# Kernel optimization log

Hardware: AMD Instinct MI355X
Metric: run time of the kernel (lower is better)

## Reference

```python
import jax, jax.numpy as jnp
import numpy as np

L = 2          # num encoder layers
D = 256        # node_dim / d_model
H = 4          # nhead
FF = 4 * D     # dim_feedforward
GEO = 8        # geo feature dim (bi ++ bj)
HID = 512      # relation MLP hidden
C = 56         # num_rel_classes
N = 384        # number of nodes


def layer_norm(x, g, b, eps=1e-5):
    mu = jnp.mean(x, axis=-1, keepdims=True)
    var = jnp.mean((x - mu) ** 2, axis=-1, keepdims=True)
    return (x - mu) * jax.lax.rsqrt(var + eps) * g + b


def encoder_layer(x, wi, bi, wo, bo, w1, b1, w2, b2, g1, be1, g2, be2):
    # Post-norm torch TransformerEncoderLayer (norm_first=False, relu)
    n = x.shape[0]
    dh = D // H
    qkv = x @ wi + bi                                  # [n, 3D]
    q, k, v = jnp.split(qkv, 3, axis=-1)
    q = q.reshape(n, H, dh)
    k = k.reshape(n, H, dh)
    v = v.reshape(n, H, dh)
    scores = jnp.einsum('nhd,mhd->hnm', q, k) * (dh ** -0.5)
    attn = jax.nn.softmax(scores, axis=-1)
    o = jnp.einsum('hnm,mhd->nhd', attn, v).reshape(n, D) @ wo + bo
    x = layer_norm(x + o, g1, be1)
    f = jax.nn.relu(x @ w1 + b1) @ w2 + b2
    x = layer_norm(x + f, g2, be2)
    return x


def setup_inputs() -> dict:
    key = jax.random.key(0)
    ks = jax.random.split(key, 16)
    s = 0.02
    f32 = jnp.float32
    return {
        'node_feats': jax.random.normal(ks[0], (N, D), f32),
        'boxes_norm': jax.random.uniform(ks[1], (N, 4), dtype=f32),
        'attn_w_in': jax.random.normal(ks[2], (L, D, 3 * D), f32) * s,
        'attn_b_in': jnp.zeros((L, 3 * D), f32),
        'attn_w_out': jax.random.normal(ks[3], (L, D, D), f32) * s,
        'attn_b_out': jnp.zeros((L, D), f32),
        'ffn_w1': jax.random.normal(ks[4], (L, D, FF), f32) * s,
        'ffn_b1': jnp.zeros((L, FF), f32),
        'ffn_w2': jax.random.normal(ks[5], (L, FF, D), f32) * s,
        'ffn_b2': jnp.zeros((L, D), f32),
        'ln1_g': jnp.ones((L, D), f32),
        'ln1_b': jnp.zeros((L, D), f32),
        'ln2_g': jnp.ones((L, D), f32),
        'ln2_b': jnp.zeros((L, D), f32),
        'mlp_w1': jax.random.normal(ks[6], (2 * D + GEO, HID), f32) * s,
        'mlp_b1': jnp.zeros((HID,), f32),
        'mlp_w2': jax.random.normal(ks[7], (HID, C), f32) * s,
        'mlp_b2': jnp.zeros((C,), f32),
    }


def reference(node_feats, boxes_norm, attn_w_in, attn_b_in, attn_w_out,
              attn_b_out, ffn_w1, ffn_b1, ffn_w2, ffn_b2, ln1_g, ln1_b,
              ln2_g, ln2_b, mlp_w1, mlp_b1, mlp_w2, mlp_b2):
    x = node_feats
    for l in range(L):
        x = encoder_layer(x, attn_w_in[l], attn_b_in[l], attn_w_out[l],
                          attn_b_out[l], ffn_w1[l], ffn_b1[l], ffn_w2[l],
                          ffn_b2[l], ln1_g[l], ln1_b[l], ln2_g[l], ln2_b[l])
    n = node_feats.shape[0]
    # all ordered pairs (i, j), i != j, in row-major order matching the loop
    i_full = np.repeat(np.arange(n), n)
    j_full = np.tile(np.arange(n), n)
    keep = i_full != j_full
    idx_i = jnp.asarray(i_full[keep])
    idx_j = jnp.asarray(j_full[keep])
    rel_in = jnp.concatenate(
        [x[idx_i], x[idx_j], boxes_norm[idx_i], boxes_norm[idx_j]], axis=1)
    rel_logits = jax.nn.relu(rel_in @ mlp_w1 + mlp_b1) @ mlp_w2 + mlp_b2
    pair_idx = jnp.stack([idx_i, idx_j], axis=1)
    return (pair_idx, rel_logits)
```

## Files before the change

### kernel.cpp

```cpp
#include <hip/hip_runtime.h>

#define NN 384
#define DM 256
#define NH 4
#define FF 1024
#define HIDN 512
#define NCLS 56
#define NPAIR (NN*(NN-1))

typedef __attribute__((ext_vector_type(8))) short short8v;
typedef __attribute__((ext_vector_type(4))) float f32x4;
typedef __attribute__((ext_vector_type(16))) float f32x16;
typedef __attribute__((ext_vector_type(8))) unsigned short ushort8;
typedef __attribute__((ext_vector_type(4))) unsigned int uint4v;

static __device__ __forceinline__ unsigned short f2bf(float f) {
  unsigned u = __float_as_uint(f);
  unsigned r = u + 0x7fff + ((u >> 16) & 1);
  return (unsigned short)(r >> 16);
}
static __device__ __forceinline__ float bf2f(unsigned short v) {
  return __uint_as_float(((unsigned)v) << 16);
}
static __device__ __forceinline__ unsigned cvt_pk_bf16(float lo, float hi) {
  unsigned r;
  asm("v_cvt_pk_bf16_f32 %0, %1, %2" : "=v"(r) : "v"(lo), "v"(hi));
  return r;
}
#define MLROW(reg, half) (((reg) & 3) + 8 * ((reg) >> 2) + 4 * (half))

__global__ __launch_bounds__(256)
void pack_all(const float* __restrict__ wi, const float* __restrict__ wo,
              const float* __restrict__ w1, const float* __restrict__ w2,
              const float* __restrict__ mw1, const float* __restrict__ mw2,
              unsigned short* __restrict__ wi_f, unsigned short* __restrict__ wo_f,
              unsigned short* __restrict__ w1_f, unsigned short* __restrict__ w2_f,
              unsigned short* __restrict__ mw1_f, unsigned short* __restrict__ mw2_f) {
  int y = blockIdx.y, z = blockIdx.z;
  int t = blockIdx.x * 256 + threadIdx.x;
  const float* src; unsigned short* dst; int K, N; long sS, sD;
  switch (y) {
    case 0: src = wi;  dst = wi_f;  K = 256;  N = 768;  sS = 256L*768;  sD = 196608; break;
    case 1: src = wo;  dst = wo_f;  K = 256;  N = 256;  sS = 256L*256;  sD = 65536;  break;
    case 2: src = w1;  dst = w1_f;  K = 256;  N = 1024; sS = 256L*1024; sD = 262144; break;
    case 3: src = w2;  dst = w2_f;  K = 1024; N = 256;  sS = 1024L*256; sD = 262144; break;
    case 4: src = mw1; dst = mw1_f; K = 256;  N = 512;  sS = 256L*512;  sD = 131072; break;
    default: {
      if (z || t >= 4096) return;
      int l = t & 63, nt = (t >> 6) & 1, ks = t >> 7;
      int kb = ks * 16 + ((l >> 5) * 8), n = nt * 32 + (l & 31);
      #pragma unroll
      for (int r = 0; r < 8; ++r) {
        float v = (n < NCLS) ? mw2[(size_t)(kb + r) * NCLS + n] : 0.f;
        mw2_f[(size_t)t * 8 + r] = f2bf(v);
      }
      return;
    }
  }
  int Nt = N >> 5;
  int total = (K >> 4) * Nt * 64;
  if (t >= total) return;
  src += z * sS; dst += z * sD;
  int l = t & 63;
  int rem = t >> 6;
  int nt = rem % Nt, ks = rem / Nt;
  int kb = ks * 16 + ((l >> 5) * 8), n = nt * 32 + (l & 31);
  #pragma unroll
  for (int r = 0; r < 8; ++r)
    dst[(size_t)t * 8 + r] = f2bf(src[(size_t)(kb + r) * N + n]);
}

__global__ __launch_bounds__(256)
void x_init(const float* __restrict__ node, float* __restrict__ xbuf,
            unsigned short* __restrict__ xbf) {
  int i = blockIdx.x * 256 + threadIdx.x;
  float v = node[i];
  xbuf[i] = v;
  xbf[i] = f2bf(v);
}

__global__ __launch_bounds__(128)
void qkv_mfma(const unsigned short* __restrict__ xbf, const unsigned short* __restrict__ wif,
              const float* __restrict__ bi, unsigned short* __restrict__ qk,
              unsigned short* __restrict__ vt) {
  int id = blockIdx.x * 2 + (threadIdx.x >> 6);
  int lane = threadIdx.x & 63;
  int mt = id % 12, nt = id / 12;
  int col = lane & 31, half = lane >> 5;
  const unsigned short* asrc = xbf + (size_t)(mt * 32 + col) * 256 + half * 8;
  const unsigned short* bsrc = wif + ((size_t)nt * 64 + lane) * 8;
  f32x16 acc = {};
  #pragma unroll
  for (int ks = 0; ks < 16; ++ks) {
    short8v a = *reinterpret_cast<const short8v*>(asrc + ks * 16);
    short8v b = *reinterpret_cast<const short8v*>(bsrc + (size_t)ks * 24 * 512);
    acc = __builtin_amdgcn_mfma_f32_32x32x16_bf16(a, b, acc, 0, 0, 0);
  }
  int n = nt * 32 + col;
  float bb = bi[n];
  #pragma unroll
  for (int reg = 0; reg < 16; ++reg) {
    int row = mt * 32 + MLROW(reg, half);
    float v = acc[reg] + bb;
    if (n < 512) qk[(size_t)row * 512 + n] = f2bf(v);
    else         vt[(size_t)(n - 512) * 384 + row] = f2bf(v);
  }
}

__global__ __launch_bounds__(256)
void fused_attn(const unsigned short* __restrict__ qk, const unsigned short* __restrict__ vt,
                unsigned short* __restrict__ attno) {
  __shared__ float S[32][385];
  __shared__ unsigned short P[32][392];
  int n0 = blockIdx.x * 32;
  int h = blockIdx.y;
  int wave = threadIdx.x >> 6, lane = threadIdx.x & 63;
  int col = lane & 31, half = lane >> 5;
  {
    const unsigned short* asrc = qk + (size_t)(n0 + col) * 512 + h * 64 + half * 8;
    #pragma unroll
    for (int jj = 0; jj < 3; ++jj) {
      int ntk = wave * 3 + jj;
      const unsigned short* bsrc = qk + (size_t)(ntk * 32 + col) * 512 + 256 + h * 64 + half * 8;
      f32x16 acc = {};
      #pragma unroll
      for (int ks = 0; ks < 4; ++ks) {
        short8v a = *reinterpret_cast<const short8v*>(asrc + ks * 16);
        short8v b = *reinterpret_cast<const short8v*>(bsrc + ks * 16);
        acc = __builtin_amdgcn_mfma_f32_32x32x16_bf16(a, b, acc, 0, 0, 0);
      }
      #pragma unroll
      for (int reg = 0; reg < 16; ++reg)
        S[MLROW(reg, half)][ntk * 32 + col] = acc[reg] * 0.125f;
    }
  }
  __syncthreads();
  {
    int row = threadIdx.x >> 3, q = threadIdx.x & 7;
    float mx = -1e30f;
    #pragma unroll 8
    for (int c = 0; c < 48; ++c) mx = fmaxf(mx, S[row][q * 48 + c]);
    mx = fmaxf(mx, __shfl_xor(mx, 1));
    mx = fmaxf(mx, __shfl_xor(mx, 2));
    mx = fmaxf(mx, __shfl_xor(mx, 4));
    float sum = 0.f;
    #pragma unroll 8
    for (int c = 0; c < 48; ++c) {
      float e = __expf(S[row][q * 48 + c] - mx);
      S[row][q * 48 + c] = e;
      sum += e;
    }
    sum += __shfl_xor(sum, 1);
    sum += __shfl_xor(sum, 2);
    sum += __shfl_xor(sum, 4);
    float inv = 1.0f / sum;
    #pragma unroll 8
    for (int c = 0; c < 48; ++c)
      P[row][q * 48 + c] = f2bf(S[row][q * 48 + c] * inv);
  }
  __syncthreads();
  if (wave < 2) {
    int ntd = wave;
    const unsigned short* bsrc = vt + (size_t)(h * 64 + ntd * 32 + col) * 384 + half * 8;
    f32x16 acc = {};
    #pragma unroll
    for (int ks = 0; ks < 24; ++ks) {
      short8v a = *reinterpret_cast<const short8v*>(&P[col][ks * 16 + half * 8]);
      short8v b = *reinterpret_cast<const short8v*>(bsrc + ks * 16);
      acc = __builtin_amdgcn_mfma_f32_32x32x16_bf16(a, b, acc, 0, 0, 0);
    }
    #pragma unroll
    for (int reg = 0; reg < 16; ++reg)
      attno[(size_t)(n0 + MLROW(reg, half)) * 256 + h * 64 + ntd * 32 + col] =
          f2bf(acc[reg]);
  }
}

__global__ __launch_bounds__(256)
void add_ln(float* __restrict__ x, unsigned short* __restrict__ xbf,
            const float* __restrict__ r,
            const float* __restrict__ g, const float* __restrict__ b) {
  int i = blockIdx.x, t = threadIdx.x;
  float v = x[(size_t)i * DM + t] + r[(size_t)i * DM + t];
  __shared__ float red[256];
  red[t] = v; __syncthreads();
  for (int s = 128; s > 0; s >>= 1) { if (t < s) red[t] += red[t + s]; __syncthreads(); }
  float mu = red[0] * (1.0f / DM); __syncthreads();
  float dv = v - mu;
  red[t] = dv * dv; __syncthreads();
  for (int s = 128; s > 0; s >>= 1) { if (t < s) red[t] += red[t + s]; __syncthreads(); }
  float var = red[0] * (1.0f / DM);
  float inv = rsqrtf(var + 1e-5f);
  float o = dv * inv * g[t] + b[t];
  x[(size_t)i * DM + t] = o;
  xbf[(size_t)i * DM + t] = f2bf(o);
}

template<int OUT_BF16, int RELU, int NKS, int NT>
__global__ void mfma_gemm(const unsigned short* __restrict__ A, int lda, long sA,
               const unsigned short* __restrict__ Bfrag, long sB,
               const float* __restrict__ bias,
               float* __restrict__ Cf, unsigned short* __restrict__ Cb,
               int ldc, long sC, int Mt) {
  int id = blockIdx.x * (blockDim.x >> 6) + (threadIdx.x >> 6);
  if (id >= Mt * NT) return;
  int lane = threadIdx.x & 63;
  int mt = id % Mt, nt = id / Mt;
  int z = blockIdx.z;
  int col = lane & 31, half = lane >> 5;
  const unsigned short* asrc = A + z * sA + (size_t)(mt * 32 + col) * lda + half * 8;
  const unsigned short* bsrc = Bfrag + z * sB + ((size_t)nt * 64 + lane) * 8;
  f32x16 acc = {};
  #pragma unroll
  for (int ks = 0; ks < NKS; ++ks) {
    short8v a = *reinterpret_cast<const short8v*>(asrc + ks * 16);
    short8v b = *reinterpret_cast<const short8v*>(bsrc + (size_t)ks * NT * 512);
    acc = __builtin_amdgcn_mfma_f32_32x32x16_bf16(a, b, acc, 0, 0, 0);
  }
  int n = nt * 32 + col;
  float bb = bias ? bias[n] : 0.f;
  #pragma unroll
  for (int reg = 0; reg < 16; ++reg) {
    int row = mt * 32 + MLROW(reg, half);
    float v = acc[reg] + bb;
    if (RELU) v = fmaxf(v, 0.f);
    if (OUT_BF16) Cb[z * sC + (size_t)row * ldc + n] = f2bf(v);
    else          Cf[z * sC + (size_t)row * ldc + n] = v;
  }
}

__global__ __launch_bounds__(128)
void uv_gemm(const unsigned short* __restrict__ xbf, const unsigned short* __restrict__ mw1f,
             const float* __restrict__ mw1, const float* __restrict__ b1,
             const float* __restrict__ boxes,
             float* __restrict__ U, unsigned short* __restrict__ Vbf) {
  int id = blockIdx.x * 2 + (threadIdx.x >> 6);
  int lane = threadIdx.x & 63;
  int z = blockIdx.z;
  int mt = id % 12, nt = id / 12;
  int col = lane & 31, half = lane >> 5;
  const unsigned short* asrc = xbf + (size_t)(mt * 32 + col) * 256 + half * 8;
  const unsigned short* bsrc = mw1f + (size_t)z * 131072 + ((size_t)nt * 64 + lane) * 8;
  f32x16 acc = {};
  #pragma unroll
  for (int ks = 0; ks < 16; ++ks) {
    short8v a = *reinterpret_cast<const short8v*>(asrc + ks * 16);
    short8v b = *reinterpret_cast<const short8v*>(bsrc + (size_t)ks * 16 * 512);
    acc = __builtin_amdgcn_mfma_f32_32x32x16_bf16(a, b, acc, 0, 0, 0);
  }
  int n = nt * 32 + col;
  float w0 = mw1[(size_t)(512 + z * 4 + 0) * HIDN + n];
  float w1r = mw1[(size_t)(512 + z * 4 + 1) * HIDN + n];
  float w2r = mw1[(size_t)(512 + z * 4 + 2) * HIDN + n];
  float w3 = mw1[(size_t)(512 + z * 4 + 3) * HIDN + n];
  float bb = (z == 0) ? b1[n] : 0.f;
  #pragma unroll
  for (int reg = 0; reg < 16; ++reg) {
    int row = mt * 32 + MLROW(reg, half);
    const float* bx = boxes + row * 4;
    float v = acc[reg] + bb + bx[0] * w0 + bx[1] * w1r + bx[2] * w2r + bx[3] * w3;
    if (z == 0) U[(size_t)row * HIDN + n] = v;
    else        Vbf[(size_t)row * HIDN + n] = f2bf(v);
  }
}

__global__ __launch_bounds__(256)
void pair_idx_kernel(float* __restrict__ out) {
  int p = blockIdx.x * 256 + threadIdx.x;
  if (p >= NPAIR) return;
  int i = p / (NN - 1);
  int r = p - i * (NN - 1);
  int j = r + (r >= i ? 1 : 0);
  out[2 * p + 0] = (float)i;
  out[2 * p + 1] = (float)j;
}

__global__ __launch_bounds__(512, 2)
void pair_mfma(const float* __restrict__ U, const unsigned short* __restrict__ Vbf,
               const unsigned short* __restrict__ w2frag,
               const float* __restrict__ b2, float* __restrict__ out) {
  __shared__ unsigned short w2l[32768];
  #pragma unroll
  for (int p = 0; p < 8; ++p) {
    int off = p * 4096 + threadIdx.x * 8;
    *reinterpret_cast<uint4v*>(&w2l[off]) =
        *reinterpret_cast<const uint4v*>(w2frag + off);
  }
  __syncthreads();

  int wave = threadIdx.x >> 6, lane = threadIdx.x & 63;
  int task = blockIdx.x * 8 + wave;
  int i = task / 12, jt = task % 12;
  int col = lane & 31, half = lane >> 5;
  int j_row = jt * 32 + col;

  const unsigned short* vsrc = Vbf + (size_t)j_row * HIDN + half * 8;
  const float* usrc = U + (size_t)i * HIDN + half * 8;
  const unsigned short* bsrc = w2l + (size_t)lane * 8;

  f32x16 acc0 = {}, acc1 = {};
  #pragma unroll
  for (int ks = 0; ks < 32; ++ks) {
    ushort8 v8 = *reinterpret_cast<const ushort8*>(vsrc + ks * 16);
    short8v b0 = *reinterpret_cast<const short8v*>(bsrc + (size_t)(ks * 2 + 0) * 512);
    short8v b1v = *reinterpret_cast<const short8v*>(bsrc + (size_t)(ks * 2 + 1) * 512);
    float4 ua = *reinterpret_cast<const float4*>(usrc + ks * 16);
    float4 ub = *reinterpret_cast<const float4*>(usrc + ks * 16 + 4);
    uint4v pk;
    pk[0] = cvt_pk_bf16(fmaxf(bf2f(v8[0]) + ua.x, 0.f), fmaxf(bf2f(v8[1]) + ua.y, 0.f));
    pk[1] = cvt_pk_bf16(fmaxf(bf2f(v8[2]) + ua.z, 0.f), fmaxf(bf2f(v8[3]) + ua.w, 0.f));
    pk[2] = cvt_pk_bf16(fmaxf(bf2f(v8[4]) + ub.x, 0.f), fmaxf(bf2f(v8[5]) + ub.y, 0.f));
    pk[3] = cvt_pk_bf16(fmaxf(bf2f(v8[6]) + ub.z, 0.f), fmaxf(bf2f(v8[7]) + ub.w, 0.f));
    short8v a = *reinterpret_cast<short8v*>(&pk);
    acc0 = __builtin_amdgcn_mfma_f32_32x32x16_bf16(a, b0, acc0, 0, 0, 0);
    acc1 = __builtin_amdgcn_mfma_f32_32x32x16_bf16(a, b1v, acc1, 0, 0, 0);
  }

  float b2v0 = b2[col];
  float b2v1 = (32 + col < NCLS) ? b2[32 + col] : 0.f;
  float* lg = out + 2 * (size_t)NPAIR;
  #pragma unroll
  for (int reg = 0; reg < 16; ++reg) {
    int j = jt * 32 + MLROW(reg, half);
    if (j != i) {
      int p = i * (NN - 1) + (j > i ? j - 1 : j);
      float* row = lg + (size_t)p * NCLS;
      row[col] = acc0[reg] + b2v0;
      if (col < NCLS - 32) row[32 + col] = acc1[reg] + b2v1;
    }
  }
}

extern "C" void kernel_launch(void* const* d_in, const int* in_sizes, int n_in,
                              void* d_out, int out_size, void* d_ws, size_t ws_size,
                              hipStream_t stream) {
  const float* node   = (const float*)d_in[0];
  const float* boxes  = (const float*)d_in[1];
  const float* w_in   = (const float*)d_in[2];
  const float* b_in   = (const float*)d_in[3];
  const float* w_out  = (const float*)d_in[4];
  const float* b_out  = (const float*)d_in[5];
  const float* fw1    = (const float*)d_in[6];
  const float* fb1    = (const float*)d_in[7];
  const float* fw2    = (const float*)d_in[8];
  const float* fb2    = (const float*)d_in[9];
  const float* ln1g   = (const float*)d_in[10];
  const float* ln1b   = (const float*)d_in[11];
  const float* ln2g   = (const float*)d_in[12];
  const float* ln2b   = (const float*)d_in[13];
  const float* mw1    = (const float*)d_in[14];
  const float* mb1    = (const float*)d_in[15];
  const float* mw2    = (const float*)d_in[16];
  const float* mb2    = (const float*)d_in[17];
  float* out = (float*)d_out;

  float* ws = (float*)d_ws;
  float* xbuf = ws;
  float* proj = xbuf + 98304;
  float* U    = proj + 98304;
  unsigned short* us = (unsigned short*)(U + 196608);
  unsigned short* x_bf   = us;             us += 98304;
  unsigned short* qk_bf  = us;             us += 196608;
  unsigned short* vt_bf  = us;             us += 98304;
  unsigned short* at_bf  = us;             us += 98304;
  unsigned short* ffh_bf = us;             us += 393216;
  unsigned short* Vbf    = us;             us += 196608;
  unsigned short* wi_f   = us;             us += 393216;
  unsigned short* wo_f   = us;             us += 131072;
  unsigned short* fw1_f  = us;             us += 524288;
  unsigned short* fw2_f  = us;             us += 524288;
  unsigned short* mw1_f  = us;             us += 262144;
  unsigned short* w2_f   = us;             us += 32768;

  pack_all<<<dim3(128, 6, 2), 256, 0, stream>>>(w_in, w_out, fw1, fw2, mw1, mw2,
                                                wi_f, wo_f, fw1_f, fw2_f, mw1_f, w2_f);
  pair_idx_kernel<<<dim3((NPAIR + 255) / 256), 256, 0, stream>>>(out);
  x_init<<<dim3(384), 256, 0, stream>>>(node, xbuf, x_bf);

  for (int l = 0; l < 2; ++l) {
    qkv_mfma<<<dim3(144), 128, 0, stream>>>(x_bf, wi_f + (size_t)l * 196608,
                                            b_in + (size_t)l * 768, qk_bf, vt_bf);
    fused_attn<<<dim3(12, 4), 256, 0, stream>>>(qk_bf, vt_bf, at_bf);
    mfma_gemm<0, 0, 16, 8><<<dim3(48), 128, 0, stream>>>(
        at_bf, 256, 0, wo_f + (size_t)l * 65536, 0, b_out + (size_t)l * 256,
        proj, nullptr, 256, 0, 12);
    add_ln<<<dim3(NN), 256, 0, stream>>>(xbuf, x_bf, proj,
                                         ln1g + (size_t)l * 256, ln1b + (size_t)l * 256);
    mfma_gemm<1, 1, 16, 32><<<dim3(192), 128, 0, stream>>>(
        x_bf, 256, 0, fw1_f + (size_t)l * 262144, 0, fb1 + (size_t)l * 1024,
        nullptr, ffh_bf, 1024, 0, 12);
    mfma_gemm<0, 0, 64, 8><<<dim3(48), 128, 0, stream>>>(
        ffh_bf, 1024, 0, fw2_f + (size_t)l * 262144, 0, fb2 + (size_t)l * 256,
        proj, nullptr, 256, 0, 12);
    add_ln<<<dim3(NN), 256, 0, stream>>>(xbuf, x_bf, proj,
                                         ln2g + (size_t)l * 256, ln2b + (size_t)l * 256);
  }

  uv_gemm<<<dim3(96, 1, 2), 128, 0, stream>>>(x_bf, mw1_f, mw1, mb1, boxes, U, Vbf);
  pair_mfma<<<dim3(576), 512, 0, stream>>>(U, Vbf, w2_f, mb2, out);
}
```

Baseline: 142.3 us.

## Read W2 fragments from global and double-buffer operand loads in pair MFMA

The pair-logit kernel no longer stages the 64KB W2 fragment table into LDS, so it drops the block-wide copy and barrier and reads B fragments straight from global memory, where they should hit in cache. The main loop is software-pipelined with two register sets so loads for step k+2 are issued while step k computes. Blocks shrink from 8 to 4 waves and the grid doubles to keep the same work split. The risk is more global and L2 traffic for W2, which every wave rereads, and higher register pressure from the double buffering.

```diff
diff --git a/kernel.cpp b/kernel.cpp
--- a/kernel.cpp
+++ b/kernel.cpp
@@ -275,46 +275,58 @@
   out[2 * p + 1] = (float)j;
 }
 
-__global__ __launch_bounds__(512, 2)
+__global__ __launch_bounds__(256, 2)
 void pair_mfma(const float* __restrict__ U, const unsigned short* __restrict__ Vbf,
                const unsigned short* __restrict__ w2frag,
                const float* __restrict__ b2, float* __restrict__ out) {
-  __shared__ unsigned short w2l[32768];
-  #pragma unroll
-  for (int p = 0; p < 8; ++p) {
-    int off = p * 4096 + threadIdx.x * 8;
-    *reinterpret_cast<uint4v*>(&w2l[off]) =
-        *reinterpret_cast<const uint4v*>(w2frag + off);
-  }
-  __syncthreads();
-
   int wave = threadIdx.x >> 6, lane = threadIdx.x & 63;
-  int task = blockIdx.x * 8 + wave;
+  int task = blockIdx.x * 4 + wave;
   int i = task / 12, jt = task % 12;
   int col = lane & 31, half = lane >> 5;
   int j_row = jt * 32 + col;
 
   const unsigned short* vsrc = Vbf + (size_t)j_row * HIDN + half * 8;
   const float* usrc = U + (size_t)i * HIDN + half * 8;
-  const unsigned short* bsrc = w2l + (size_t)lane * 8;
+  const unsigned short* bsrc = w2frag + (size_t)lane * 8;
 
   f32x16 acc0 = {}, acc1 = {};
-  #pragma unroll
-  for (int ks = 0; ks < 32; ++ks) {
-    ushort8 v8 = *reinterpret_cast<const ushort8*>(vsrc + ks * 16);
-    short8v b0 = *reinterpret_cast<const short8v*>(bsrc + (size_t)(ks * 2 + 0) * 512);
-    short8v b1v = *reinterpret_cast<const short8v*>(bsrc + (size_t)(ks * 2 + 1) * 512);
-    float4 ua = *reinterpret_cast<const float4*>(usrc + ks * 16);
-    float4 ub = *reinterpret_cast<const float4*>(usrc + ks * 16 + 4);
-    uint4v pk;
-    pk[0] = cvt_pk_bf16(fmaxf(bf2f(v8[0]) + ua.x, 0.f), fmaxf(bf2f(v8[1]) + ua.y, 0.f));
-    pk[1] = cvt_pk_bf16(fmaxf(bf2f(v8[2]) + ua.z, 0.f), fmaxf(bf2f(v8[3]) + ua.w, 0.f));
-    pk[2] = cvt_pk_bf16(fmaxf(bf2f(v8[4]) + ub.x, 0.f), fmaxf(bf2f(v8[5]) + ub.y, 0.f));
-    pk[3] = cvt_pk_bf16(fmaxf(bf2f(v8[6]) + ub.z, 0.f), fmaxf(bf2f(v8[7]) + ub.w, 0.f));
-    short8v a = *reinterpret_cast<short8v*>(&pk);
-    acc0 = __builtin_amdgcn_mfma_f32_32x32x16_bf16(a, b0, acc0, 0, 0, 0);
-    acc1 = __builtin_amdgcn_mfma_f32_32x32x16_bf16(a, b1v, acc1, 0, 0, 0);
-  }
+
+  short8v b0a, b1a, b0b, b1b;
+  ushort8 v8a, v8b;
+  float4 uaa, uba, uab, ubb;
+
+#define PLOAD(ks, B0, B1, V8, UA, UB) do {                                         \
+    B0 = *reinterpret_cast<const short8v*>(bsrc + (size_t)((ks) * 2 + 0) * 512);   \
+    B1 = *reinterpret_cast<const short8v*>(bsrc + (size_t)((ks) * 2 + 1) * 512);   \
+    V8 = *reinterpret_cast<const ushort8*>(vsrc + (ks) * 16);                      \
+    UA = *reinterpret_cast<const float4*>(usrc + (ks) * 16);                       \
+    UB = *reinterpret_cast<const float4*>(usrc + (ks) * 16 + 4); } while (0)
+
+#define PCOMP(B0, B1, V8, UA, UB) do {                                             \
+    uint4v pk;                                                                     \
+    pk[0] = cvt_pk_bf16(fmaxf(bf2f(V8[0]) + UA.x, 0.f),                            \
+                        fmaxf(bf2f(V8[1]) + UA.y, 0.f));                           \
+    pk[1] = cvt_pk_bf16(fmaxf(bf2f(V8[2]) + UA.z, 0.f),                            \
+                        fmaxf(bf2f(V8[3]) + UA.w, 0.f));                           \
+    pk[2] = cvt_pk_bf16(fmaxf(bf2f(V8[4]) + UB.x, 0.f),                            \
+                        fmaxf(bf2f(V8[5]) + UB.y, 0.f));                           \
+    pk[3] = cvt_pk_bf16(fmaxf(bf2f(V8[6]) + UB.z, 0.f),                            \
+                        fmaxf(bf2f(V8[7]) + UB.w, 0.f));                           \
+    short8v a = *reinterpret_cast<short8v*>(&pk);                                  \
+    acc0 = __builtin_amdgcn_mfma_f32_32x32x16_bf16(a, B0, acc0, 0, 0, 0);          \
+    acc1 = __builtin_amdgcn_mfma_f32_32x32x16_bf16(a, B1, acc1, 0, 0, 0); } while (0)
+
+  PLOAD(0, b0a, b1a, v8a, uaa, uba);
+  PLOAD(1, b0b, b1b, v8b, uab, ubb);
+  #pragma unroll
+  for (int ks = 0; ks < 32; ks += 2) {
+    PCOMP(b0a, b1a, v8a, uaa, uba);
+    if (ks + 2 < 32) PLOAD(ks + 2, b0a, b1a, v8a, uaa, uba);
+    PCOMP(b0b, b1b, v8b, uab, ubb);
+    if (ks + 3 < 32) PLOAD(ks + 3, b0b, b1b, v8b, uab, ubb);
+  }
+#undef PLOAD
+#undef PCOMP
 
   float b2v0 = b2[col];
   float b2v1 = (32 + col < NCLS) ? b2[32 + col] : 0.f;
@@ -397,5 +409,5 @@
   }
 
   uv_gemm<<<dim3(96, 1, 2), 128, 0, stream>>>(x_bf, mw1_f, mw1, mb1, boxes, U, Vbf);
-  pair_mfma<<<dim3(576), 512, 0, stream>>>(U, Vbf, w2_f, mb2, out);
-}
+  pair_mfma<<<dim3(1152), 256, 0, stream>>>(U, Vbf, w2_f, mb2, out);
+}
```

Result: slower. 145.4 us (+2.1%).
